# Performance work log

Hardware: AMD Instinct MI355X
Metric: run time of the kernel (lower is better)

The kernel has to match this reference:

```python
import jax, jax.numpy as jnp
import numpy as np

CURVATURE = 1.0
EPS_DENOM = 1e-06
BALL_SCALE = 0.1  # keep points inside the Poincare ball


def setup_inputs() -> dict:
    key = jax.random.key(0)
    k1, k2 = jax.random.split(key)
    B, H, N, D = 2, 8, 2048, 64
    q = jax.random.normal(k1, (B, H, N, D), dtype=jnp.float32) * BALL_SCALE
    k = jax.random.normal(k2, (B, H, N, D), dtype=jnp.float32) * BALL_SCALE
    return {"q": q, "k": k}


def reference(q, k):
    c = CURVATURE
    # squared norms: [B,H,N]
    q_norm_sq = jnp.sum(q * q, axis=-1)
    k_norm_sq = jnp.sum(k * k, axis=-1)
    # pairwise squared distance via quadratic expansion (avoids O(N^2*D) diff tensor)
    # diff_sq[b,h,i,j] = |q_i|^2 + |k_j|^2 - 2 q_i.k_j
    qk = jnp.einsum('bhid,bhjd->bhij', q, k)
    diff_sq = q_norm_sq[..., :, None] + k_norm_sq[..., None, :] - 2.0 * qk
    diff_sq = jnp.maximum(diff_sq, 0.0)  # guard fp roundoff
    denom = (1.0 - c * q_norm_sq)[..., :, None] * (1.0 - c * k_norm_sq)[..., None, :]
    denom = jnp.maximum(denom, EPS_DENOM)
    cosh_arg = 1.0 + 2.0 * c * diff_sq / denom
    cosh_arg = jnp.maximum(cosh_arg, 1.0)
    return jnp.arccosh(cosh_arg)
```

## Files before the change

kernel.cpp:

```cpp
#include <hip/hip_runtime.h>

#define N_SEQ 2048
#define D_DIM 64
#define BH_CNT 16
#define TILE 64
#define LDSTR 72
#define TSTR 68

typedef __attribute__((ext_vector_type(8))) short bf16x8;
typedef __attribute__((ext_vector_type(4))) float f32x4;

__device__ __forceinline__ short f2bf(float f) {
  union { float f; unsigned u; } v; v.f = f;
  unsigned r = v.u + 0x7FFFu + ((v.u >> 16) & 1u);
  return (short)(r >> 16);
}

__device__ __forceinline__ float hyp_dist(float qns, float kns, float qk) {
  float diff  = fmaxf(qns + kns - 2.0f * qk, 0.0f);
  float denom = fmaxf((1.0f - qns) * (1.0f - kns), 1e-6f);
  float t2 = __fdividef(2.0f * diff, denom);
  float s  = __builtin_amdgcn_sqrtf(t2 * (t2 + 2.0f));
  return __logf(1.0f + t2 + s);
}

__global__ void __launch_bounds__(256)
hyp_kernel(const float* __restrict__ qg,
           const float* __restrict__ kg,
           float* __restrict__ out)
{
  __shared__ __align__(16) char smem_raw[TILE * LDSTR * 2 * sizeof(short)];
  __shared__ float qn_s[TILE];
  __shared__ float kn_s[TILE];
  short* Qs = (short*)smem_raw;
  short* Ks = Qs + TILE * LDSTR;
  float* Ts = (float*)smem_raw;

  const int t  = threadIdx.x;
  const int bh = blockIdx.z;
  const int ti = blockIdx.y;
  const int tj = blockIdx.x;

  const int row  = t >> 2;
  const int part = t & 3;
  const float* gq = qg + ((size_t)bh * N_SEQ + (size_t)ti * TILE) * D_DIM;
  const float* gk = kg + ((size_t)bh * N_SEQ + (size_t)tj * TILE) * D_DIM;
#pragma unroll
  for (int m = 0; m < 2; ++m) {
    const float* g = (m ? gk : gq) + row * D_DIM + part * 16;
    short* lds     = (m ? Ks : Qs) + row * LDSTR + part * 16;
    float* nrm     = m ? kn_s : qn_s;
    float4 v0 = ((const float4*)g)[0];
    float4 v1 = ((const float4*)g)[1];
    float4 v2 = ((const float4*)g)[2];
    float4 v3 = ((const float4*)g)[3];
    float p = v0.x*v0.x + v0.y*v0.y + v0.z*v0.z + v0.w*v0.w
            + v1.x*v1.x + v1.y*v1.y + v1.z*v1.z + v1.w*v1.w
            + v2.x*v2.x + v2.y*v2.y + v2.z*v2.z + v2.w*v2.w
            + v3.x*v3.x + v3.y*v3.y + v3.z*v3.z + v3.w*v3.w;
    p += __shfl_xor(p, 1);
    p += __shfl_xor(p, 2);
    if (part == 0) nrm[row] = p;
    bf16x8 pk0, pk1;
    pk0[0]=f2bf(v0.x); pk0[1]=f2bf(v0.y); pk0[2]=f2bf(v0.z); pk0[3]=f2bf(v0.w);
    pk0[4]=f2bf(v1.x); pk0[5]=f2bf(v1.y); pk0[6]=f2bf(v1.z); pk0[7]=f2bf(v1.w);
    pk1[0]=f2bf(v2.x); pk1[1]=f2bf(v2.y); pk1[2]=f2bf(v2.z); pk1[3]=f2bf(v2.w);
    pk1[4]=f2bf(v3.x); pk1[5]=f2bf(v3.y); pk1[6]=f2bf(v3.z); pk1[7]=f2bf(v3.w);
    ((bf16x8*)lds)[0] = pk0;
    ((bf16x8*)lds)[1] = pk1;
  }
  __syncthreads();

  const int lane = t & 63;
  const int wv   = t >> 6;
  const int wj   = (wv & 1) * 32;
  const int wi   = (wv >> 1) * 32;
  const int l15  = lane & 15;
  const int quad = lane >> 4;

  const f32x4 zero = {0.0f, 0.0f, 0.0f, 0.0f};
  f32x4 acc[2][2];
#pragma unroll
  for (int a = 0; a < 2; ++a)
#pragma unroll
    for (int b = 0; b < 2; ++b)
      acc[a][b] = zero;

#pragma unroll
  for (int s = 0; s < 2; ++s) {
    const int koff = s * 32 + quad * 8;
    bf16x8 fa[2], fb[2];
#pragma unroll
    for (int mj = 0; mj < 2; ++mj)
      fa[mj] = *(const bf16x8*)&Ks[(wj + mj * 16 + l15) * LDSTR + koff];
#pragma unroll
    for (int ni = 0; ni < 2; ++ni)
      fb[ni] = *(const bf16x8*)&Qs[(wi + ni * 16 + l15) * LDSTR + koff];
#pragma unroll
    for (int mj = 0; mj < 2; ++mj)
#pragma unroll
      for (int ni = 0; ni < 2; ++ni)
        acc[mj][ni] = __builtin_amdgcn_mfma_f32_16x16x32_bf16(
            fa[mj], fb[ni], acc[mj][ni], 0, 0, 0);
  }

  __syncthreads();

#pragma unroll
  for (int mj = 0; mj < 2; ++mj) {
    const int jl = wj + mj * 16 + quad * 4;
    const float4 kn4 = *(const float4*)&kn_s[jl];
#pragma unroll
    for (int ni = 0; ni < 2; ++ni) {
      const int il = wi + ni * 16 + l15;
      const float qns = qn_s[il];
      f32x4 a4 = acc[mj][ni];
      f32x4 res;
      res[0] = hyp_dist(qns, kn4.x, a4[0]);
      res[1] = hyp_dist(qns, kn4.y, a4[1]);
      res[2] = hyp_dist(qns, kn4.z, a4[2]);
      res[3] = hyp_dist(qns, kn4.w, a4[3]);
      *(f32x4*)&Ts[il * TSTR + jl] = res;
    }
  }
  __syncthreads();

  float* outb = out + (size_t)bh * N_SEQ * N_SEQ
                    + (size_t)(ti * TILE) * N_SEQ + tj * TILE;
  const int l  = t & 15;
  const int rq = t >> 4;
#pragma unroll
  for (int p = 0; p < 4; ++p) {
    const int r = p * 16 + rq;
    f32x4 v = *(const f32x4*)&Ts[r * TSTR + 4 * l];
    *(f32x4*)(outb + (size_t)r * N_SEQ + 4 * l) = v;
  }
}

extern "C" void kernel_launch(void* const* d_in, const int* in_sizes, int n_in,
                              void* d_out, int out_size, void* d_ws, size_t ws_size,
                              hipStream_t stream) {
  const float* q = (const float*)d_in[0];
  const float* k = (const float*)d_in[1];
  float* out = (float*)d_out;
  dim3 grid(N_SEQ / TILE, N_SEQ / TILE, BH_CNT);
  hyp_kernel<<<grid, 256, 0, stream>>>(q, k, out);
}
```

Baseline: 316.8 us.

## Widen output tile to 64x256 per block and stage stores in two halves

Each block now computes a 64x256 tile instead of 64x64. Every wave owns 64 K-columns across all 64 Q rows with a 4x4 MFMA accumulator grid. This cuts the block count and the redundant loading and bf16 conversion of Q and K tiles. The output is staged through LDS in two 32-row halves so each wave writes full 1 KB contiguous row segments, at the cost of more registers per thread and lower occupancy.

```diff
diff --git a/kernel.cpp b/kernel.cpp
--- a/kernel.cpp
+++ b/kernel.cpp
@@ -3,9 +3,10 @@
 #define N_SEQ 2048
 #define D_DIM 64
 #define BH_CNT 16
-#define TILE 64
+#define TI 64
+#define TJ 256
 #define LDSTR 72
-#define TSTR 68
+#define TSTR 260
 
 typedef __attribute__((ext_vector_type(8))) short bf16x8;
 typedef __attribute__((ext_vector_type(4))) float f32x4;
@@ -29,11 +30,11 @@
            const float* __restrict__ kg,
            float* __restrict__ out)
 {
-  __shared__ __align__(16) char smem_raw[TILE * LDSTR * 2 * sizeof(short)];
-  __shared__ float qn_s[TILE];
-  __shared__ float kn_s[TILE];
+  __shared__ __align__(16) char smem_raw[(TI + TJ) * LDSTR * sizeof(short)];
+  __shared__ __align__(16) float qn_s[TI];
+  __shared__ __align__(16) float kn_s[TJ];
   short* Qs = (short*)smem_raw;
-  short* Ks = Qs + TILE * LDSTR;
+  short* Ks = Qs + TI * LDSTR;
   float* Ts = (float*)smem_raw;
 
   const int t  = threadIdx.x;
@@ -43,13 +44,14 @@
 
   const int row  = t >> 2;
   const int part = t & 3;
-  const float* gq = qg + ((size_t)bh * N_SEQ + (size_t)ti * TILE) * D_DIM;
-  const float* gk = kg + ((size_t)bh * N_SEQ + (size_t)tj * TILE) * D_DIM;
+  const float* gq = qg + ((size_t)bh * N_SEQ + (size_t)ti * TI) * D_DIM;
+  const float* gk = kg + ((size_t)bh * N_SEQ + (size_t)tj * TJ) * D_DIM;
 #pragma unroll
-  for (int m = 0; m < 2; ++m) {
-    const float* g = (m ? gk : gq) + row * D_DIM + part * 16;
-    short* lds     = (m ? Ks : Qs) + row * LDSTR + part * 16;
-    float* nrm     = m ? kn_s : qn_s;
+  for (int m = 0; m < 5; ++m) {
+    const int r64  = (m == 0) ? row : (m - 1) * 64 + row;
+    const float* g = ((m == 0) ? gq : gk) + r64 * D_DIM + part * 16;
+    short* lds     = ((m == 0) ? Qs : Ks) + r64 * LDSTR + part * 16;
+    float* nrm     = (m == 0) ? (qn_s + r64) : (kn_s + r64);
     float4 v0 = ((const float4*)g)[0];
     float4 v1 = ((const float4*)g)[1];
     float4 v2 = ((const float4*)g)[2];
@@ -60,7 +62,7 @@
             + v3.x*v3.x + v3.y*v3.y + v3.z*v3.z + v3.w*v3.w;
     p += __shfl_xor(p, 1);
     p += __shfl_xor(p, 2);
-    if (part == 0) nrm[row] = p;
+    if (part == 0) *nrm = p;
     bf16x8 pk0, pk1;
     pk0[0]=f2bf(v0.x); pk0[1]=f2bf(v0.y); pk0[2]=f2bf(v0.z); pk0[3]=f2bf(v0.w);
     pk0[4]=f2bf(v1.x); pk0[5]=f2bf(v1.y); pk0[6]=f2bf(v1.z); pk0[7]=f2bf(v1.w);
@@ -73,46 +75,43 @@
 
   const int lane = t & 63;
   const int wv   = t >> 6;
-  const int wj   = (wv & 1) * 32;
-  const int wi   = (wv >> 1) * 32;
+  const int wj   = wv * 64;
   const int l15  = lane & 15;
   const int quad = lane >> 4;
 
   const f32x4 zero = {0.0f, 0.0f, 0.0f, 0.0f};
-  f32x4 acc[2][2];
+  f32x4 acc[4][4];
 #pragma unroll
-  for (int a = 0; a < 2; ++a)
+  for (int a = 0; a < 4; ++a)
 #pragma unroll
-    for (int b = 0; b < 2; ++b)
+    for (int b = 0; b < 4; ++b)
       acc[a][b] = zero;
 
 #pragma unroll
   for (int s = 0; s < 2; ++s) {
     const int koff = s * 32 + quad * 8;
-    bf16x8 fa[2], fb[2];
+    bf16x8 fa[4], fb[4];
 #pragma unroll
-    for (int mj = 0; mj < 2; ++mj)
+    for (int mj = 0; mj < 4; ++mj)
       fa[mj] = *(const bf16x8*)&Ks[(wj + mj * 16 + l15) * LDSTR + koff];
 #pragma unroll
-    for (int ni = 0; ni < 2; ++ni)
-      fb[ni] = *(const bf16x8*)&Qs[(wi + ni * 16 + l15) * LDSTR + koff];
+    for (int ni = 0; ni < 4; ++ni)
+      fb[ni] = *(const bf16x8*)&Qs[(ni * 16 + l15) * LDSTR + koff];
 #pragma unroll
-    for (int mj = 0; mj < 2; ++mj)
+    for (int mj = 0; mj < 4; ++mj)
 #pragma unroll
-      for (int ni = 0; ni < 2; ++ni)
+      for (int ni = 0; ni < 4; ++ni)
         acc[mj][ni] = __builtin_amdgcn_mfma_f32_16x16x32_bf16(
             fa[mj], fb[ni], acc[mj][ni], 0, 0, 0);
   }
 
-  __syncthreads();
-
 #pragma unroll
-  for (int mj = 0; mj < 2; ++mj) {
+  for (int mj = 0; mj < 4; ++mj) {
     const int jl = wj + mj * 16 + quad * 4;
     const float4 kn4 = *(const float4*)&kn_s[jl];
 #pragma unroll
-    for (int ni = 0; ni < 2; ++ni) {
-      const int il = wi + ni * 16 + l15;
+    for (int ni = 0; ni < 4; ++ni) {
+      const int il = ni * 16 + l15;
       const float qns = qn_s[il];
       f32x4 a4 = acc[mj][ni];
       f32x4 res;
@@ -120,20 +119,32 @@
       res[1] = hyp_dist(qns, kn4.y, a4[1]);
       res[2] = hyp_dist(qns, kn4.z, a4[2]);
       res[3] = hyp_dist(qns, kn4.w, a4[3]);
-      *(f32x4*)&Ts[il * TSTR + jl] = res;
+      acc[mj][ni] = res;
     }
   }
-  __syncthreads();
 
   float* outb = out + (size_t)bh * N_SEQ * N_SEQ
-                    + (size_t)(ti * TILE) * N_SEQ + tj * TILE;
-  const int l  = t & 15;
-  const int rq = t >> 4;
+                    + (size_t)(ti * TI) * N_SEQ + (size_t)tj * TJ;
 #pragma unroll
-  for (int p = 0; p < 4; ++p) {
-    const int r = p * 16 + rq;
-    f32x4 v = *(const f32x4*)&Ts[r * TSTR + 4 * l];
-    *(f32x4*)(outb + (size_t)r * N_SEQ + 4 * l) = v;
+  for (int c = 0; c < 2; ++c) {
+    __syncthreads();
+#pragma unroll
+    for (int mj = 0; mj < 4; ++mj) {
+      const int jl = wj + mj * 16 + quad * 4;
+#pragma unroll
+      for (int nn = 0; nn < 2; ++nn) {
+        const int ni = 2 * c + nn;
+        const int rr = nn * 16 + l15;
+        *(f32x4*)&Ts[rr * TSTR + jl] = acc[mj][ni];
+      }
+    }
+    __syncthreads();
+#pragma unroll
+    for (int p = 0; p < 8; ++p) {
+      const int r = p * 4 + wv;
+      f32x4 v = *(const f32x4*)&Ts[r * TSTR + lane * 4];
+      *(f32x4*)(outb + (size_t)(c * 32 + r) * N_SEQ + lane * 4) = v;
+    }
   }
 }
 
@@ -143,6 +154,6 @@
   const float* q = (const float*)d_in[0];
   const float* k = (const float*)d_in[1];
   float* out = (float*)d_out;
-  dim3 grid(N_SEQ / TILE, N_SEQ / TILE, BH_CNT);
+  dim3 grid(N_SEQ / TJ, N_SEQ / TI, BH_CNT);
   hyp_kernel<<<grid, 256, 0, stream>>>(q, k, out);
 }
```

Result: slower. 336.6 us (+6.2%).

## Precompute bf16 operands and per-row norm terms in a prep kernel

Applied to the files above, without the earlier changes.

Adds a prep kernel that converts q and k to bf16 once and stores per-row terms (2|x|^2, 1-|x|^2, its reciprocal) in workspace. The main kernel then loads half-size bf16 tiles and the precomputed terms instead of re-reading and re-converting fp32 rows in every tile block. The epilogue is also reformulated to use a reciprocal product instead of a division and computes acosh directly via log2. This adds an extra launch and workspace traffic, and keeps the old kernel as a fallback when the workspace is too small.

```diff
diff --git a/kernel.cpp b/kernel.cpp
--- a/kernel.cpp
+++ b/kernel.cpp
@@ -7,6 +7,9 @@
 #define LDSTR 72
 #define TSTR 68
 
+#define WS_NEED 9437184ull
+#define NROWS   32768
+
 typedef __attribute__((ext_vector_type(8))) short bf16x8;
 typedef __attribute__((ext_vector_type(4))) float f32x4;
 
@@ -16,7 +19,160 @@
   return (short)(r >> 16);
 }
 
-__device__ __forceinline__ float hyp_dist(float qns, float kns, float qk) {
+__global__ void __launch_bounds__(256)
+prep_kernel(const float* __restrict__ qg, const float* __restrict__ kg,
+            short* __restrict__ qbf, short* __restrict__ kbf,
+            float4* __restrict__ qrow, float4* __restrict__ krow)
+{
+  const int b = blockIdx.x;
+  const int t = threadIdx.x;
+  const int tensor = b >> 10;
+  const float* src = tensor ? kg : qg;
+  short* dbf       = tensor ? kbf : qbf;
+  float4* drow     = tensor ? krow : qrow;
+
+  const int r   = (b & 1023) * 32 + (t >> 3);
+  const int sub = t & 7;
+  const size_t e = (size_t)r * 64 + sub * 8;
+
+  float4 v0 = ((const float4*)(src + e))[0];
+  float4 v1 = ((const float4*)(src + e))[1];
+  float p = v0.x*v0.x + v0.y*v0.y + v0.z*v0.z + v0.w*v0.w
+          + v1.x*v1.x + v1.y*v1.y + v1.z*v1.z + v1.w*v1.w;
+  p += __shfl_xor(p, 1);
+  p += __shfl_xor(p, 2);
+  p += __shfl_xor(p, 4);
+
+  bf16x8 pk;
+  pk[0]=f2bf(v0.x); pk[1]=f2bf(v0.y); pk[2]=f2bf(v0.z); pk[3]=f2bf(v0.w);
+  pk[4]=f2bf(v1.x); pk[5]=f2bf(v1.y); pk[6]=f2bf(v1.z); pk[7]=f2bf(v1.w);
+  *(bf16x8*)&dbf[e] = pk;
+
+  if (sub == 0) {
+    float a = 1.0f - p;
+    drow[r] = make_float4(2.0f * p, a, 1.0f / a, 0.0f);
+  }
+}
+
+__global__ void __launch_bounds__(256)
+hyp_main(const short* __restrict__ qbf, const short* __restrict__ kbf,
+         const float4* __restrict__ qrow, const float4* __restrict__ krow,
+         float* __restrict__ out)
+{
+  __shared__ __align__(16) char smem_raw[TILE * LDSTR * 2 * sizeof(short)];
+  __shared__ __align__(16) float q2s[TILE], as_[TILE], ras[TILE];
+  __shared__ __align__(16) float k2s[TILE], bs_[TILE], rbs[TILE];
+  short* Qs = (short*)smem_raw;
+  short* Ks = Qs + TILE * LDSTR;
+  float* Ts = (float*)smem_raw;
+
+  const int t  = threadIdx.x;
+  const int bh = blockIdx.z;
+  const int ti = blockIdx.y;
+  const int tj = blockIdx.x;
+  const int qrb = bh * N_SEQ + ti * TILE;
+  const int krb = bh * N_SEQ + tj * TILE;
+
+  const int srow = t >> 3;
+  const int scol = (t & 7) * 8;
+#pragma unroll
+  for (int p = 0; p < 2; ++p) {
+    const int r = srow + p * 32;
+    *(bf16x8*)&Qs[r * LDSTR + scol] =
+        *(const bf16x8*)&qbf[(size_t)(qrb + r) * 64 + scol];
+    *(bf16x8*)&Ks[r * LDSTR + scol] =
+        *(const bf16x8*)&kbf[(size_t)(krb + r) * 64 + scol];
+  }
+  if (t < 64) {
+    float4 v = qrow[qrb + t];
+    q2s[t] = v.x; as_[t] = v.y; ras[t] = v.z;
+  } else if (t < 128) {
+    const int u = t - 64;
+    float4 v = krow[krb + u];
+    k2s[u] = v.x; bs_[u] = v.y; rbs[u] = v.z;
+  }
+  __syncthreads();
+
+  const int lane = t & 63;
+  const int wv   = t >> 6;
+  const int wj   = (wv & 1) * 32;
+  const int wi   = (wv >> 1) * 32;
+  const int l15  = lane & 15;
+  const int quad = lane >> 4;
+
+  const f32x4 zero = {0.0f, 0.0f, 0.0f, 0.0f};
+  f32x4 acc[2][2];
+#pragma unroll
+  for (int a = 0; a < 2; ++a)
+#pragma unroll
+    for (int b = 0; b < 2; ++b)
+      acc[a][b] = zero;
+
+#pragma unroll
+  for (int s = 0; s < 2; ++s) {
+    const int koff = s * 32 + quad * 8;
+    bf16x8 fa[2], fb[2];
+#pragma unroll
+    for (int mj = 0; mj < 2; ++mj)
+      fa[mj] = *(const bf16x8*)&Ks[(wj + mj * 16 + l15) * LDSTR + koff];
+#pragma unroll
+    for (int ni = 0; ni < 2; ++ni)
+      fb[ni] = *(const bf16x8*)&Qs[(wi + ni * 16 + l15) * LDSTR + koff];
+#pragma unroll
+    for (int mj = 0; mj < 2; ++mj)
+#pragma unroll
+      for (int ni = 0; ni < 2; ++ni)
+        acc[mj][ni] = __builtin_amdgcn_mfma_f32_16x16x32_bf16(
+            fa[mj], fb[ni], acc[mj][ni], 0, 0, 0);
+  }
+
+  __syncthreads();
+
+#pragma unroll
+  for (int mj = 0; mj < 2; ++mj) {
+    const int jl = wj + mj * 16 + quad * 4;
+    const float4 k2v = *(const float4*)&k2s[jl];
+    const float4 bv  = *(const float4*)&bs_[jl];
+    const float4 rbv = *(const float4*)&rbs[jl];
+    const float* k2p = (const float*)&k2v;
+    const float* bp  = (const float*)&bv;
+    const float* rbp = (const float*)&rbv;
+#pragma unroll
+    for (int ni = 0; ni < 2; ++ni) {
+      const int il = wi + ni * 16 + l15;
+      const float q2  = q2s[il];
+      const float av  = as_[il];
+      const float rav = ras[il];
+      f32x4 a4 = acc[mj][ni];
+      f32x4 res;
+#pragma unroll
+      for (int j = 0; j < 4; ++j) {
+        float n    = fmaxf(fmaf(-4.0f, a4[j], q2 + k2p[j]), 0.0f);
+        float prod = av * bp[j];
+        float iv   = rav * rbp[j];
+        iv = (prod > 1e-6f) ? iv : 1e6f;
+        float x = fmaf(n, iv, 1.0f);
+        float s = __builtin_amdgcn_sqrtf(fmaf(x, x, -1.0f));
+        res[j] = __log2f(x + s) * 0.6931471805599453f;
+      }
+      *(f32x4*)&Ts[il * TSTR + jl] = res;
+    }
+  }
+  __syncthreads();
+
+  float* outb = out + (size_t)bh * N_SEQ * N_SEQ
+                    + (size_t)(ti * TILE) * N_SEQ + tj * TILE;
+  const int l  = t & 15;
+  const int rq = t >> 4;
+#pragma unroll
+  for (int p = 0; p < 4; ++p) {
+    const int r = p * 16 + rq;
+    f32x4 v = *(const f32x4*)&Ts[r * TSTR + 4 * l];
+    *(f32x4*)(outb + (size_t)r * N_SEQ + 4 * l) = v;
+  }
+}
+
+__device__ __forceinline__ float hyp_dist_fb(float qns, float kns, float qk) {
   float diff  = fmaxf(qns + kns - 2.0f * qk, 0.0f);
   float denom = fmaxf((1.0f - qns) * (1.0f - kns), 1e-6f);
   float t2 = __fdividef(2.0f * diff, denom);
@@ -25,9 +181,8 @@
 }
 
 __global__ void __launch_bounds__(256)
-hyp_kernel(const float* __restrict__ qg,
-           const float* __restrict__ kg,
-           float* __restrict__ out)
+hyp_fb(const float* __restrict__ qg, const float* __restrict__ kg,
+       float* __restrict__ out)
 {
   __shared__ __align__(16) char smem_raw[TILE * LDSTR * 2 * sizeof(short)];
   __shared__ float qn_s[TILE];
@@ -116,10 +271,10 @@
       const float qns = qn_s[il];
       f32x4 a4 = acc[mj][ni];
       f32x4 res;
-      res[0] = hyp_dist(qns, kn4.x, a4[0]);
-      res[1] = hyp_dist(qns, kn4.y, a4[1]);
-      res[2] = hyp_dist(qns, kn4.z, a4[2]);
-      res[3] = hyp_dist(qns, kn4.w, a4[3]);
+      res[0] = hyp_dist_fb(qns, kn4.x, a4[0]);
+      res[1] = hyp_dist_fb(qns, kn4.y, a4[1]);
+      res[2] = hyp_dist_fb(qns, kn4.z, a4[2]);
+      res[3] = hyp_dist_fb(qns, kn4.w, a4[3]);
       *(f32x4*)&Ts[il * TSTR + jl] = res;
     }
   }
@@ -144,5 +299,15 @@
   const float* k = (const float*)d_in[1];
   float* out = (float*)d_out;
   dim3 grid(N_SEQ / TILE, N_SEQ / TILE, BH_CNT);
-  hyp_kernel<<<grid, 256, 0, stream>>>(q, k, out);
-}
+
+  if (ws_size >= WS_NEED && d_ws != nullptr) {
+    short* qbf  = (short*)d_ws;
+    short* kbf  = qbf + 2097152;
+    float4* qrow = (float4*)((char*)d_ws + 8388608);
+    float4* krow = qrow + NROWS;
+    prep_kernel<<<dim3(2048, 1, 1), 256, 0, stream>>>(q, k, qbf, kbf, qrow, krow);
+    hyp_main<<<grid, 256, 0, stream>>>(qbf, kbf, qrow, krow, out);
+  } else {
+    hyp_fb<<<grid, 256, 0, stream>>>(q, k, out);
+  }
+}
```

New measurement: 285.1 us. 10.0% less time.
